# Kernel tuning notes

Measured on AMD Instinct MI355X. Metric: run time of the kernel, lower is better.

The kernel has to match this reference:

```python
import jax, jax.numpy as jnp
import numpy as np

EMBED_DIM = 1024
NUM_HEADS = 16
HEAD_DIM = EMBED_DIM // NUM_HEADS


def setup_inputs() -> dict:
    key = jax.random.key(0)
    ks = jax.random.split(key, 5)
    B, S, D = 2, 2048, EMBED_DIM
    scale = 1.0 / np.sqrt(D)
    x = jax.random.normal(ks[0], (B, S, D), dtype=jnp.float32)
    qkv_w = jax.random.uniform(ks[1], (3 * D, D), dtype=jnp.float32, minval=-scale, maxval=scale)
    qkv_b = jax.random.uniform(ks[2], (3 * D,), dtype=jnp.float32, minval=-scale, maxval=scale)
    out_w = jax.random.uniform(ks[3], (D, D), dtype=jnp.float32, minval=-scale, maxval=scale)
    out_b = jax.random.uniform(ks[4], (D,), dtype=jnp.float32, minval=-scale, maxval=scale)
    return {"x": x, "qkv_w": qkv_w, "qkv_b": qkv_b, "out_w": out_w, "out_b": out_b}


def reference(x, qkv_w, qkv_b, out_w, out_b):
    B, S, D = x.shape
    H, hd = NUM_HEADS, HEAD_DIM
    # QKV projection (torch Linear: y = x @ W^T + b)
    qkv = jnp.einsum('bsd,ed->bse', x, qkv_w) + qkv_b          # [B,S,3D]
    qkv = qkv.reshape(B, S, 3, H, hd)
    q, k, v = (jnp.moveaxis(qkv[:, :, i], 2, 1) for i in range(3))  # each [B,H,S,hd]
    scores = jnp.einsum('bhqd,bhkd->bhqk', q, k) / np.sqrt(hd)  # [B,H,S,S]
    probs = jax.nn.softmax(scores, axis=-1)
    attn = jnp.einsum('bhqk,bhkd->bhqd', probs, v)              # [B,H,S,hd]
    attn = jnp.moveaxis(attn, 1, 2).reshape(B, S, D)
    return jnp.einsum('bsd,ed->bse', attn, out_w) + out_b
```

## Files before the change

### kernel.cpp

```cpp
#include <hip/hip_runtime.h>
#include <stdint.h>

typedef __bf16 bf16;
typedef __attribute__((ext_vector_type(2))) __bf16 bf16x2;
typedef __attribute__((ext_vector_type(4))) __bf16 bf16x4;
typedef __attribute__((ext_vector_type(8))) __bf16 bf16x8;
typedef __attribute__((ext_vector_type(4))) float f32x4;
typedef __attribute__((ext_vector_type(16))) float f32x16;

#define LOG2E_OVER_8 0.18033688011112042f

#if __has_builtin(__builtin_amdgcn_exp2f)
#define EXP2(x) __builtin_amdgcn_exp2f(x)
#else
#define EXP2(x) exp2f(x)
#endif

__device__ __forceinline__ void gl_lds16(const bf16* g, bf16* l) {
  __builtin_amdgcn_global_load_lds(
      (const __attribute__((address_space(1))) void*)g,
      (__attribute__((address_space(3))) void*)l, 16, 0, 0);
}
#define WAIT_VM0_BARRIER() asm volatile("s_waitcnt vmcnt(0)\n\ts_barrier" ::: "memory")

__device__ __forceinline__ uint32_t pack2(float a, float b) {
  union { bf16x2 v; uint32_t u; } z;
  z.v[0] = (bf16)a; z.v[1] = (bf16)b;
  return z.u;
}

__device__ __forceinline__ void pl32swap(uint32_t& a, uint32_t& b) {
  asm("v_permlane32_swap_b32 %0, %1" : "+v"(a), "+v"(b));
}

#define N_X  (4096 * 1024)
#define N_WQ (3072 * 1024)
#define N_WO (1024 * 1024)
__global__ __launch_bounds__(256) void cvt3_kernel(const float* __restrict__ x,
                                                   const float* __restrict__ wq,
                                                   const float* __restrict__ wo,
                                                   bf16* __restrict__ d) {
  int i = (blockIdx.x * 256 + threadIdx.x) * 8;
  const float* s;
  if (i < N_X) s = x + i;
  else if (i < N_X + N_WQ) s = wq + (i - N_X);
  else s = wo + (i - N_X - N_WQ);
  float4 a = *(const float4*)s;
  float4 b = *(const float4*)(s + 4);
  bf16x8 o;
  o[0] = (bf16)a.x; o[1] = (bf16)a.y; o[2] = (bf16)a.z; o[3] = (bf16)a.w;
  o[4] = (bf16)b.x; o[5] = (bf16)b.y; o[6] = (bf16)b.z; o[7] = (bf16)b.w;
  *(bf16x8*)(d + i) = o;
}

template <int EPI>
__global__ __launch_bounds__(256, 3) void gemm_bt(
    const bf16* __restrict__ A, const bf16* __restrict__ Bw,
    const float* __restrict__ bias,
    bf16* __restrict__ qo, bf16* __restrict__ ko, bf16* __restrict__ vTo,
    float* __restrict__ outF) {
  constexpr int MT = EPI ? 64 : 128;
  constexpr int MI = MT / 32;
  constexpr int BK = EPI ? 64 : 32;
  constexpr int NC = BK / 32;
  constexpr int NIT = 1024 / BK;
  constexpr int ASZ = MT * BK;
  constexpr int BSZ = 128 * BK;
  constexpr int RS = 136;
  constexpr int SME0 = 2 * ASZ + 2 * BSZ;
  constexpr int SME = EPI ? SME0 : (SME0 > 128 * RS ? SME0 : 128 * RS);
  __shared__ __attribute__((aligned(16))) bf16 smem[SME];

  int bx, by;
  {
    const int f = blockIdx.x;
    const int xcd = f & 7, idx = f >> 3;
    if constexpr (EPI == 0) { by = xcd * 4 + (idx & 3); bx = idx >> 2; }
    else                    { by = xcd * 8 + (idx & 7); bx = idx >> 3; }
  }

  const int t = threadIdx.x;
  const int L = t & 63;
  const int li = L & 15;
  const int qd = L >> 4;
  const int w = t >> 6;
  const int wm = (w >> 1) * (MT / 2);
  const int wn = (w & 1) * 64;
  const int bm0 = by * MT;
  const int bn0 = bx * 128;
  const int r_st = t >> 2;
  const int c_st = (t & 3) * 8;

  const bf16* Ab = A + (size_t)bm0 * 1024;
  const bf16* Bb = Bw + (size_t)bn0 * 1024;

  auto issue = [&](int k0, int bi) {
    bf16* As_ = smem + bi * ASZ;
    bf16* Bs_ = smem + 2 * ASZ + bi * BSZ;
#pragma unroll
    for (int kc = 0; kc < NC; ++kc) {
      const int kk = k0 + kc * 32;
      gl_lds16(Ab + (size_t)r_st * 1024 + kk + c_st, As_ + kc * MT * 32 + t * 8);
      if constexpr (MT == 128)
        gl_lds16(Ab + (size_t)(r_st + 64) * 1024 + kk + c_st,
                 As_ + kc * MT * 32 + (t + 256) * 8);
      gl_lds16(Bb + (size_t)r_st * 1024 + kk + c_st, Bs_ + kc * 4096 + t * 8);
      gl_lds16(Bb + (size_t)(r_st + 64) * 1024 + kk + c_st,
               Bs_ + kc * 4096 + (t + 256) * 8);
    }
  };

  f32x4 acc[MI][4] = {};
  issue(0, 0);
  for (int it = 0; it < NIT; ++it) {
    WAIT_VM0_BARRIER();
    if (it < NIT - 1) issue((it + 1) * BK, (it + 1) & 1);
    const bf16* Ac = smem + (it & 1) * ASZ;
    const bf16* Bc = smem + 2 * ASZ + (it & 1) * BSZ;
#pragma unroll
    for (int kc = 0; kc < NC; ++kc) {
      const bf16* Ak = Ac + kc * MT * 32;
      const bf16* Bk = Bc + kc * 4096;
      bf16x8 af[MI], bfr[4];
#pragma unroll
      for (int mi = 0; mi < MI; ++mi)
        af[mi] = *(const bf16x8*)(Ak + (wm + mi * 16 + li) * 32 + qd * 8);
#pragma unroll
      for (int ni = 0; ni < 4; ++ni)
        bfr[ni] = *(const bf16x8*)(Bk + (wn + ni * 16 + li) * 32 + qd * 8);
#pragma unroll
      for (int mi = 0; mi < MI; ++mi)
#pragma unroll
        for (int ni = 0; ni < 4; ++ni)
          acc[mi][ni] = __builtin_amdgcn_mfma_f32_16x16x32_bf16(
              af[mi], bfr[ni], acc[mi][ni], 0, 0, 0);
    }
  }

  if constexpr (EPI == 0) {
    const int which = bn0 >> 10;
    __syncthreads();
    bf16* Ct = smem;
    if (which == 2) {
#pragma unroll
      for (int mi = 0; mi < MI; ++mi) {
        const int m_l = wm + mi * 16 + qd * 4;
#pragma unroll
        for (int ni = 0; ni < 4; ++ni) {
          const int n_l = wn + ni * 16 + li;
          const float bi = bias[bn0 + n_l];
          bf16x4 pk;
#pragma unroll
          for (int r = 0; r < 4; ++r) pk[r] = (bf16)(acc[mi][ni][r] + bi);
          *(bf16x4*)(Ct + n_l * RS + m_l) = pk;
        }
      }
    } else {
      const float sc = (which == 0) ? LOG2E_OVER_8 : 1.0f;
#pragma unroll
      for (int mi = 0; mi < MI; ++mi) {
        const int m_l = wm + mi * 16 + qd * 4;
#pragma unroll
        for (int ni = 0; ni < 4; ++ni) {
          const int n_l = wn + ni * 16 + li;
          const float bi = bias[bn0 + n_l];
#pragma unroll
          for (int r = 0; r < 4; ++r)
            Ct[(m_l + r) * RS + n_l] = (bf16)((acc[mi][ni][r] + bi) * sc);
        }
      }
    }
    __syncthreads();
    const int jr = t >> 4;
    const int jc = t & 15;
#pragma unroll
    for (int pass = 0; pass < 8; ++pass) {
      const int row = pass * 16 + jr;
      bf16x8 vv = *(const bf16x8*)(Ct + row * RS + jc * 8);
      if (which == 2) {
        const int n_g = bn0 + row;
        const int hh = (n_g >> 6) & 15, dd = n_g & 63;
        const int bb = bm0 >> 11;
        const int s_b = (bm0 & 2047) + jc * 8;
        *(bf16x8*)(vTo + ((size_t)(bb * 16 + hh) * 64 + dd) * 2048 + s_b) = vv;
      } else {
        const int m_g = bm0 + row;
        const int bb = m_g >> 11, ss = m_g & 2047;
        const int n_g = bn0 + jc * 8;
        const int hh = (n_g >> 6) & 15, dd = n_g & 63;
        bf16* dst = (which == 0 ? qo : ko);
        *(bf16x8*)(dst + ((size_t)(bb * 16 + hh) * 2048 + ss) * 64 + dd) = vv;
      }
    }
  } else {
#pragma unroll
    for (int mi = 0; mi < MI; ++mi) {
      const int m_g = bm0 + wm + mi * 16 + qd * 4;
#pragma unroll
      for (int ni = 0; ni < 4; ++ni) {
        const int n_g = bn0 + wn + ni * 16 + li;
        const float bi = bias[n_g];
#pragma unroll
        for (int r = 0; r < 4; ++r)
          outF[(size_t)(m_g + r) * 1024 + n_g] = acc[mi][ni][r] + bi;
      }
    }
  }
}

__global__ __launch_bounds__(256, 1) void attn_fwd(
    const bf16* __restrict__ Q, const bf16* __restrict__ K,
    const bf16* __restrict__ VT, bf16* __restrict__ AO) {
  __shared__ __attribute__((aligned(16))) bf16 Ks[2 * 8192];
  __shared__ __attribute__((aligned(16))) bf16 Vs[2 * 8192];
  const int t = threadIdx.x;
  const int L = t & 63;
  const int m31 = L & 31;
  const int hi = L >> 5;
  const int w = t >> 6;

  const int lid = blockIdx.x;
  const int bh_ = ((lid & 7) << 2) + (lid >> 6);
  const int qb = (lid >> 3) & 7;
  const int b = bh_ >> 4, h = bh_ & 15;
  const size_t bh = (size_t)(b * 16 + h);

  const bf16* Qp = Q + bh * 2048 * 64;
  const bf16* Kp = K + bh * 2048 * 64;
  const bf16* Vp = VT + bh * 64 * 2048;
  const int q0 = qb * 256 + w * 64;

  bf16x8 qf[2][4];
#pragma unroll
  for (int qs = 0; qs < 2; ++qs)
#pragma unroll
    for (int s = 0; s < 4; ++s)
      qf[qs][s] = *(const bf16x8*)(
          Qp + (size_t)(q0 + qs * 32 + m31) * 64 + s * 16 + hi * 8);

  f32x16 acc[2][2] = {};
  float ls[2][2] = {};

  const int srow = t >> 3;
  const int scc = (t & 7) ^ (srow & 7);
  auto issue = [&](int it2, int bi) {
#pragma unroll
    for (int tile = 0; tile < 2; ++tile) {
      const int kt = it2 * 2 + tile;
      const bf16* Kt = Kp + (size_t)kt * 4096;
      const bf16* Vt = Vp + kt * 64;
      bf16* Kd = Ks + bi * 8192 + tile * 4096;
      bf16* Vd = Vs + bi * 8192 + tile * 4096;
#pragma unroll
      for (int r = 0; r < 2; ++r) {
        gl_lds16(Kt + (srow + 32 * r) * 64 + scc * 8, Kd + (t + 256 * r) * 8);
        gl_lds16(Vt + (size_t)(srow + 32 * r) * 2048 + scc * 8, Vd + (t + 256 * r) * 8);
      }
    }
  };

  const int rlow = m31 & 7;
  union FU { uint32_t u[4]; bf16x8 v; };

  issue(0, 0);
  for (int it2 = 0; it2 < 16; ++it2) {
    WAIT_VM0_BARRIER();
    if (it2 < 15) issue(it2 + 1, (it2 + 1) & 1);
    const bf16* Kc0 = Ks + (it2 & 1) * 8192;
    const bf16* Vc0 = Vs + (it2 & 1) * 8192;

    auto QKT = [&](int kt, f32x16* st2) {
      const bf16* Kc = Kc0 + (kt >> 1) * 4096;
      bf16x8 kf[4];
#pragma unroll
      for (int s = 0; s < 4; ++s)
        kf[s] = *(const bf16x8*)(
            Kc + (((kt & 1) * 32 + m31) * 8 + ((2 * s + hi) ^ rlow)) * 8);
      __builtin_amdgcn_s_setprio(1);
#pragma unroll
      for (int qs = 0; qs < 2; ++qs) {
        f32x16 z = {};
#pragma unroll
        for (int s = 0; s < 4; ++s)
          z = __builtin_amdgcn_mfma_f32_32x32x16_bf16(kf[s], qf[qs][s], z, 0, 0, 0);
        st2[qs] = z;
      }
      __builtin_amdgcn_s_setprio(0);
    };

    auto SM = [&](const f32x16& st, int qs, int kt, FU* afp) {
      uint32_t pk[8];
      float lsl = 0.f;
#pragma unroll
      for (int j = 0; j < 8; ++j) {
        float a = EXP2(st[2 * j]);
        float c = EXP2(st[2 * j + 1]);
        lsl += a + c;
        pk[j] = pack2(a, c);
      }
      ls[qs][kt & 1] += lsl;
      pl32swap(pk[0], pk[2]);
      pl32swap(pk[1], pk[3]);
      pl32swap(pk[4], pk[6]);
      pl32swap(pk[5], pk[7]);
      afp[0].u[0] = pk[0]; afp[0].u[1] = pk[1];
      afp[0].u[2] = pk[2]; afp[0].u[3] = pk[3];
      afp[1].u[0] = pk[4]; afp[1].u[1] = pk[5];
      afp[1].u[2] = pk[6]; afp[1].u[3] = pk[7];
    };

    auto PV = [&](int kt, FU A[2][2]) {
      const bf16* Vc = Vc0 + (kt >> 1) * 4096;
      __builtin_amdgcn_s_setprio(1);
#pragma unroll
      for (int dt = 0; dt < 2; ++dt)
#pragma unroll
        for (int u = 0; u < 2; ++u) {
          bf16x8 vf = *(const bf16x8*)(
              Vc + ((dt * 32 + m31) * 8 + (((kt & 1) * 4 + u * 2 + hi) ^ rlow)) * 8);
#pragma unroll
          for (int qs = 0; qs < 2; ++qs)
            acc[dt][qs] = __builtin_amdgcn_mfma_f32_32x32x16_bf16(
                A[qs][u].v, vf, acc[dt][qs], 0, 0, 0);
        }
      __builtin_amdgcn_s_setprio(0);
    };

    f32x16 stc[2], stn[2];
    QKT(0, stc);
#pragma unroll
    for (int kt = 0; kt < 4; ++kt) {
      if (kt < 3) QKT(kt + 1, stn);
      FU A[2][2];
      SM(stc[0], 0, kt, A[0]);
      SM(stc[1], 1, kt, A[1]);
      PV(kt, A);
      stc[0] = stn[0];
      stc[1] = stn[1];
    }
  }

  float inv[2];
#pragma unroll
  for (int qs = 0; qs < 2; ++qs) {
    float l = ls[qs][0] + ls[qs][1];
    l += __shfl_xor(l, 32);
    inv[qs] = 1.f / l;
  }

#pragma unroll
  for (int qs = 0; qs < 2; ++qs)
#pragma unroll
    for (int r = 0; r < 16; ++r) {
      const int qrow = (r & 3) + 8 * (r >> 2) + 4 * hi;
      const float invq = __shfl(inv[qs], qrow);
      const size_t base =
          ((size_t)b * 2048 + q0 + qs * 32 + qrow) * 1024 + h * 64 + m31;
      AO[base] = (bf16)(acc[0][qs][r] * invq);
      AO[base + 32] = (bf16)(acc[1][qs][r] * invq);
    }
}

extern "C" void kernel_launch(void* const* d_in, const int* in_sizes, int n_in,
                              void* d_out, int out_size, void* d_ws, size_t ws_size,
                              hipStream_t stream) {
  const float* x = (const float*)d_in[0];
  const float* qkvw = (const float*)d_in[1];
  const float* qkvb = (const float*)d_in[2];
  const float* outw = (const float*)d_in[3];
  const float* outb = (const float*)d_in[4];
  float* out = (float*)d_out;

  bf16* xb = (bf16*)d_ws;
  bf16* wq = xb + (size_t)N_X;
  bf16* wo = wq + (size_t)N_WQ;
  bf16* q = wo + (size_t)N_WO;
  bf16* kk = q + (size_t)2 * 16 * 2048 * 64;
  bf16* vT = kk + (size_t)2 * 16 * 2048 * 64;
  bf16* attn = xb;

  cvt3_kernel<<<4096, 256, 0, stream>>>(x, qkvw, outw, xb);

  gemm_bt<0><<<768, 256, 0, stream>>>(xb, wq, qkvb, q, kk, vT, nullptr);
  attn_fwd<<<256, 256, 0, stream>>>(q, kk, vT, attn);
  gemm_bt<1><<<512, 256, 0, stream>>>(attn, wo, outb, nullptr, nullptr, nullptr, out);
}
```

Measured before the change: 182.9 us.

## Split key range across two half-blocks in attention and merge partials via LDS

Doubles the attention block to 512 threads. Each 256-thread half streams its own half of the key/value sequence into a separate LDS region, so the main loop runs half as many iterations. After the loop, the upper half writes its unnormalized accumulators and row sums to LDS, and the lower half adds them in, normalizes and stores the output. The goal is to raise the number of waves per CU and shorten the serial key loop, which was poorly occupied at one 4-wave block per CU. The costs are an LDS exchange step and tighter register pressure from the 512,2 launch bound, which may cause spills. The merge is a plain sum, which is only correct because the softmax carries no per-half running max.

New measurement: 172.4 us. 5.8% less time.

```diff
diff --git a/kernel.cpp b/kernel.cpp
--- a/kernel.cpp
+++ b/kernel.cpp
@@ -208,16 +208,17 @@
   }
 }
 
-__global__ __launch_bounds__(256, 1) void attn_fwd(
+__global__ __launch_bounds__(512, 2) void attn_fwd(
     const bf16* __restrict__ Q, const bf16* __restrict__ K,
     const bf16* __restrict__ VT, bf16* __restrict__ AO) {
-  __shared__ __attribute__((aligned(16))) bf16 Ks[2 * 8192];
-  __shared__ __attribute__((aligned(16))) bf16 Vs[2 * 8192];
+  __shared__ __attribute__((aligned(16))) bf16 smem[65536];
   const int t = threadIdx.x;
+  const int half = t >> 8;
+  const int tt = t & 255;
   const int L = t & 63;
   const int m31 = L & 31;
-  const int hi = L >> 5;
-  const int w = t >> 6;
+  const int hi = (L >> 5) & 1;
+  const int w = (t >> 6) & 3;
 
   const int lid = blockIdx.x;
   const int bh_ = ((lid & 7) << 2) + (lid >> 6);
@@ -226,8 +227,8 @@
   const size_t bh = (size_t)(b * 16 + h);
 
   const bf16* Qp = Q + bh * 2048 * 64;
-  const bf16* Kp = K + bh * 2048 * 64;
-  const bf16* Vp = VT + bh * 64 * 2048;
+  const bf16* Kp = K + bh * 2048 * 64 + (size_t)half * 1024 * 64;
+  const bf16* Vp = VT + bh * 64 * 2048 + half * 1024;
   const int q0 = qb * 256 + w * 64;
 
   bf16x8 qf[2][4];
@@ -241,20 +242,23 @@
   f32x16 acc[2][2] = {};
   float ls[2][2] = {};
 
-  const int srow = t >> 3;
-  const int scc = (t & 7) ^ (srow & 7);
+  bf16* Kbase = smem + half * 32768;
+  bf16* Vbase = Kbase + 16384;
+
+  const int srow = tt >> 3;
+  const int scc = (tt & 7) ^ (srow & 7);
   auto issue = [&](int it2, int bi) {
 #pragma unroll
     for (int tile = 0; tile < 2; ++tile) {
       const int kt = it2 * 2 + tile;
       const bf16* Kt = Kp + (size_t)kt * 4096;
       const bf16* Vt = Vp + kt * 64;
-      bf16* Kd = Ks + bi * 8192 + tile * 4096;
-      bf16* Vd = Vs + bi * 8192 + tile * 4096;
+      bf16* Kd = Kbase + bi * 8192 + tile * 4096;
+      bf16* Vd = Vbase + bi * 8192 + tile * 4096;
 #pragma unroll
       for (int r = 0; r < 2; ++r) {
-        gl_lds16(Kt + (srow + 32 * r) * 64 + scc * 8, Kd + (t + 256 * r) * 8);
-        gl_lds16(Vt + (size_t)(srow + 32 * r) * 2048 + scc * 8, Vd + (t + 256 * r) * 8);
+        gl_lds16(Kt + (srow + 32 * r) * 64 + scc * 8, Kd + (tt + 256 * r) * 8);
+        gl_lds16(Vt + (size_t)(srow + 32 * r) * 2048 + scc * 8, Vd + (tt + 256 * r) * 8);
       }
     }
   };
@@ -263,11 +267,11 @@
   union FU { uint32_t u[4]; bf16x8 v; };
 
   issue(0, 0);
-  for (int it2 = 0; it2 < 16; ++it2) {
+  for (int it2 = 0; it2 < 8; ++it2) {
     WAIT_VM0_BARRIER();
-    if (it2 < 15) issue(it2 + 1, (it2 + 1) & 1);
-    const bf16* Kc0 = Ks + (it2 & 1) * 8192;
-    const bf16* Vc0 = Vs + (it2 & 1) * 8192;
+    if (it2 < 7) issue(it2 + 1, (it2 + 1) & 1);
+    const bf16* Kc0 = Kbase + (it2 & 1) * 8192;
+    const bf16* Vc0 = Vbase + (it2 & 1) * 8192;
 
     auto QKT = [&](int kt, f32x16* st2) {
       const bf16* Kc = Kc0 + (kt >> 1) * 4096;
@@ -340,25 +344,51 @@
     }
   }
 
-  float inv[2];
-#pragma unroll
-  for (int qs = 0; qs < 2; ++qs) {
-    float l = ls[qs][0] + ls[qs][1];
-    l += __shfl_xor(l, 32);
-    inv[qs] = 1.f / l;
-  }
-
-#pragma unroll
-  for (int qs = 0; qs < 2; ++qs)
-#pragma unroll
-    for (int r = 0; r < 16; ++r) {
-      const int qrow = (r & 3) + 8 * (r >> 2) + 4 * hi;
-      const float invq = __shfl(inv[qs], qrow);
-      const size_t base =
-          ((size_t)b * 2048 + q0 + qs * 32 + qrow) * 1024 + h * 64 + m31;
-      AO[base] = (bf16)(acc[0][qs][r] * invq);
-      AO[base + 32] = (bf16)(acc[1][qs][r] * invq);
-    }
+  __syncthreads();
+  float* xch = (float*)smem;
+  const int slot = w * 64 + L;
+  float* rec = xch + slot * 66;
+  if (half == 1) {
+#pragma unroll
+    for (int dt = 0; dt < 2; ++dt)
+#pragma unroll
+      for (int qs = 0; qs < 2; ++qs)
+#pragma unroll
+        for (int r = 0; r < 16; ++r)
+          rec[dt * 32 + qs * 16 + r] = acc[dt][qs][r];
+    rec[64] = ls[0][0] + ls[0][1];
+    rec[65] = ls[1][0] + ls[1][1];
+  }
+  __syncthreads();
+  if (half == 0) {
+#pragma unroll
+    for (int dt = 0; dt < 2; ++dt)
+#pragma unroll
+      for (int qs = 0; qs < 2; ++qs)
+#pragma unroll
+        for (int r = 0; r < 16; ++r)
+          acc[dt][qs][r] += rec[dt * 32 + qs * 16 + r];
+
+    float inv[2];
+#pragma unroll
+    for (int qs = 0; qs < 2; ++qs) {
+      float l = ls[qs][0] + ls[qs][1] + rec[64 + qs];
+      l += __shfl_xor(l, 32);
+      inv[qs] = 1.f / l;
+    }
+
+#pragma unroll
+    for (int qs = 0; qs < 2; ++qs)
+#pragma unroll
+      for (int r = 0; r < 16; ++r) {
+        const int qrow = (r & 3) + 8 * (r >> 2) + 4 * hi;
+        const float invq = __shfl(inv[qs], qrow);
+        const size_t base =
+            ((size_t)b * 2048 + q0 + qs * 32 + qrow) * 1024 + h * 64 + m31;
+        AO[base] = (bf16)(acc[0][qs][r] * invq);
+        AO[base + 32] = (bf16)(acc[1][qs][r] * invq);
+      }
+  }
 }
 
 extern "C" void kernel_launch(void* const* d_in, const int* in_sizes, int n_in,
@@ -382,6 +412,6 @@
   cvt3_kernel<<<4096, 256, 0, stream>>>(x, qkvw, outw, xb);
 
   gemm_bt<0><<<768, 256, 0, stream>>>(xb, wq, qkvb, q, kk, vT, nullptr);
-  attn_fwd<<<256, 256, 0, stream>>>(q, kk, vT, attn);
+  attn_fwd<<<256, 512, 0, stream>>>(q, kk, vT, attn);
   gemm_bt<1><<<512, 256, 0, stream>>>(attn, wo, outb, nullptr, nullptr, nullptr, out);
 }
```
